# Kernel tuning notes

Measured on AMD Instinct MI355X. Metric: run time of the kernel, lower is better.

## Reference

```python
import jax, jax.numpy as jnp
import numpy as np

C_IN = 64       # in_channels
D = 2 * C_IN    # inner dim d = 128
D4 = 4 * D      # 4-direction SSM dim = 512
N = 16          # SSM state size
DR = 4          # delta_rank = ceil(64/16)
K = 3           # d_conv
B_SZ, H, W = 4, 64, 64
LN_EPS = 1e-5


def setup_inputs() -> dict:
    key = jax.random.key(0)
    ks = jax.random.split(key, 8)
    s = lambda k, shape, sc: jax.random.normal(k, shape, jnp.float32) * sc
    x = jax.random.normal(ks[0], (B_SZ, C_IN, H, W), jnp.float32)
    in_proj_w = s(ks[1], (2 * D, C_IN), 0.05)
    in_proj_b = jnp.zeros((2 * D,), jnp.float32)
    conv_w = s(ks[2], (D, 1, K, K), 0.1)          # depthwise OIHW, groups=D
    conv_b = jnp.zeros((D,), jnp.float32)
    x_proj_w = s(ks[3], (DR + 2 * N, D4), 0.05)   # no bias
    delta_proj_w = s(ks[4], (D4, DR), 0.1)
    delta_proj_b = s(ks[5], (D4,), 0.1)
    A_log = jnp.log(jnp.broadcast_to(jnp.arange(1, N + 1, dtype=jnp.float32), (D4, N)))
    D_param = jnp.ones((D4,), jnp.float32)
    ln_g = jnp.ones((D,), jnp.float32)
    ln_b = jnp.zeros((D,), jnp.float32)
    out_proj_w = s(ks[6], (C_IN, D), 0.05)        # no bias
    return dict(x=x, in_proj_w=in_proj_w, in_proj_b=in_proj_b, conv_w=conv_w,
                conv_b=conv_b, x_proj_w=x_proj_w, delta_proj_w=delta_proj_w,
                delta_proj_b=delta_proj_b, A_log=A_log, D_param=D_param,
                ln_g=ln_g, ln_b=ln_b, out_proj_w=out_proj_w)


def _forward(x, in_proj_w, in_proj_b, conv_w, conv_b, x_proj_w, delta_proj_w,
             delta_proj_b, A_log, D_param, ln_g, ln_b, out_proj_w):
    b, c, h, w = x.shape
    l = h * w
    # in_proj on channels-last, split into x-branch and gate z
    xz = jnp.einsum('bchw,ec->bhwe', x, in_proj_w) + in_proj_b   # (b,h,w,2D)
    xs, z = jnp.split(xz, 2, axis=-1)                             # (b,h,w,D) each
    # depthwise conv (padding 1 == SAME for k=3) + SiLU
    xc = xs.transpose(0, 3, 1, 2)                                 # (b,D,h,w)
    xc = jax.lax.conv_general_dilated(
        xc, conv_w, (1, 1), 'SAME', feature_group_count=D,
        dimension_numbers=('NCHW', 'OIHW', 'NCHW')) + conv_b[None, :, None, None]
    xc = jax.nn.silu(xc)
    # 4 scan directions: row-major, col-major, and their reversals
    x1 = xc.reshape(b, D, l)
    x2 = xc.transpose(0, 1, 3, 2).reshape(b, D, l)                # (w h) order
    xf = xc[:, :, ::-1, ::-1]
    x3 = xf.reshape(b, D, l)
    x4 = xf.transpose(0, 1, 3, 2).reshape(b, D, l)
    u = jnp.concatenate([x1, x2, x3, x4], axis=1).transpose(0, 2, 1)  # (b,l,D4)
    # input-dependent SSM params
    x_dbl = u @ x_proj_w.T                                        # (b,l,DR+2N)
    dlt, Bm, Cm = jnp.split(x_dbl, [DR, DR + N], axis=-1)
    delta = jax.nn.softplus(dlt @ delta_proj_w.T + delta_proj_b)  # (b,l,D4)
    A = -jnp.exp(A_log)                                           # (D4,N)
    # selective scan: h_t = exp(delta_t*A)*h_{t-1} + delta_t*B_t*u_t ; y_t = C_t.h_t
    def step(hst, inp):
        d_t, B_t, C_t, u_t = inp                                  # (b,D4),(b,N),(b,N),(b,D4)
        dA = jnp.exp(d_t[:, :, None] * A[None])                   # (b,D4,N)
        hst = dA * hst + (d_t * u_t)[:, :, None] * B_t[:, None, :]
        y = jnp.einsum('bdn,bn->bd', hst, C_t)
        return hst, y
    h0 = jnp.zeros((b, D4, N), x.dtype)
    xs_seq = (delta.transpose(1, 0, 2), Bm.transpose(1, 0, 2),
              Cm.transpose(1, 0, 2), u.transpose(1, 0, 2))
    _, ys = jax.lax.scan(step, h0, xs_seq)                        # (l,b,D4)
    y = ys.transpose(1, 0, 2) + u * D_param                       # (b,l,D4)
    # split directions and undo each scan ordering
    y = y.reshape(b, l, 4, D).transpose(0, 2, 3, 1)               # (b,4,D,l)
    y1 = y[:, 0].reshape(b, D, h, w)
    y2 = y[:, 1].reshape(b, D, w, h).transpose(0, 1, 3, 2)
    y3 = y[:, 2].reshape(b, D, h, w)[:, :, ::-1, ::-1]
    y4 = y[:, 3].reshape(b, D, w, h).transpose(0, 1, 3, 2)[:, :, ::-1, ::-1]
    ysum = (y1 + y2 + y3 + y4).transpose(0, 2, 3, 1)              # (b,h,w,D)
    # LayerNorm over D, gate with silu(z), out projection
    mu = ysum.mean(-1, keepdims=True)
    var = ysum.var(-1, keepdims=True)
    yn = (ysum - mu) / jnp.sqrt(var + LN_EPS) * ln_g + ln_b
    out = (yn * jax.nn.silu(z)) @ out_proj_w.T                    # (b,h,w,C_IN)
    return out.transpose(0, 3, 1, 2)                              # (b,c,h,w)


def reference(x, in_proj_w, in_proj_b, conv_w, conv_b, x_proj_w, delta_proj_w,
              delta_proj_b, A_log, D_param, ln_g, ln_b, out_proj_w):
    return _forward(x, in_proj_w, in_proj_b, conv_w, conv_b, x_proj_w,
                    delta_proj_w, delta_proj_b, A_log, D_param, ln_g, ln_b,
                    out_proj_w)
```

## Files before the change

### kernel.cpp

```cpp
#include <hip/hip_runtime.h>
#include <math.h>


#define LL   4096
#define NCH  128
#define TCH  32

__device__ __forceinline__ int tauf(int t) { return ((t & 63) << 6) | (t >> 6); }

__global__ __launch_bounds__(256) void k_inproj(const float* __restrict__ x,
    const float* __restrict__ W, const float* __restrict__ bias,
    float* __restrict__ xsl, float* __restrict__ zl)
{
    int tid = threadIdx.x;
    int b   = blockIdx.x >> 8;
    int p0  = (blockIdx.x & 255) << 4;
    int e   = tid;

    float wr[64];
    {
        const float4* wrow = (const float4*)(W + (e << 6));
        #pragma unroll
        for (int k = 0; k < 16; ++k) ((float4*)wr)[k] = wrow[k];
    }
    float acc[16];
    float bv = bias[e];
    #pragma unroll
    for (int j = 0; j < 16; ++j) acc[j] = bv;

    const float* xb = x + ((b << 6) << 12) + p0;
    #pragma unroll
    for (int c = 0; c < 64; ++c) {
        const float* xr = xb + (c << 12);
        float w = wr[c];
        #pragma unroll
        for (int j = 0; j < 16; ++j) acc[j] += w * xr[j];
    }

    float* dst = (e < 128) ? xsl : zl;
    int ch = e & 127;
    #pragma unroll
    for (int j = 0; j < 16; ++j)
        dst[(((b << 12) + p0 + j) << 7) + ch] = acc[j];
}

__global__ __launch_bounds__(256) void k_conv(const float* __restrict__ xsl,
    const float* __restrict__ cw, const float* __restrict__ cb,
    float* __restrict__ xcl)
{
    __shared__ float wlds[1152];
    int tid = threadIdx.x;
    for (int i = tid; i < 1152; i += 256) wlds[i] = cw[i];
    int c    = tid & 127, half = tid >> 7;
    int P0   = blockIdx.x << 3;
    int b    = P0 >> 12;
    int p0   = (P0 & 4095) + (half << 2);
    int r    = p0 >> 6, c0 = p0 & 63;
    __syncthreads();

    float w[9];
    #pragma unroll
    for (int k = 0; k < 9; ++k) w[k] = wlds[c * 9 + k];
    float bv = cb[c];
    float acc[4] = {bv, bv, bv, bv};

    #pragma unroll
    for (int dy = -1; dy <= 1; ++dy) {
        int rr = r + dy;
        if ((unsigned)rr < 64u) {
            float v[6];
            #pragma unroll
            for (int o = 0; o < 6; ++o) {
                int cc = c0 + o - 1;
                v[o] = ((unsigned)cc < 64u)
                     ? xsl[(((b << 12) + (rr << 6) + cc) << 7) + c] : 0.f;
            }
            int wb = (dy + 1) * 3;
            #pragma unroll
            for (int j = 0; j < 4; ++j)
                acc[j] += w[wb] * v[j] + w[wb + 1] * v[j + 1] + w[wb + 2] * v[j + 2];
        }
    }
    #pragma unroll
    for (int j = 0; j < 4; ++j) {
        float a = acc[j];
        xcl[(((b << 12) + p0 + j) << 7) + c] = a / (1.f + __expf(-a));
    }
}

__global__ __launch_bounds__(576) void k_pgemm(const float* __restrict__ xcl,
    const float* __restrict__ xpw, float* __restrict__ P)
{
    __shared__ float ut[16][128];
    __shared__ float res[16][144];
    int tid = threadIdx.x;
    int q4  = tid & 3;
    int jj  = tid >> 2;
    int r0  = blockIdx.x << 4;

    if (tid < 512) {
        int row = tid >> 5, v = tid & 31;
        ((float4*)ut[row])[v] = ((const float4*)xcl)[((r0 + row) << 5) + v];
    }

    int j = jj % 36, g = jj / 36;
    const float4* wrow = (const float4*)(xpw + j * 512 + g * 128 + q4 * 32);
    float4 wreg[8];
    #pragma unroll
    for (int k = 0; k < 8; ++k) wreg[k] = wrow[k];

    __syncthreads();

    #pragma unroll 4
    for (int row = 0; row < 16; ++row) {
        const float4* ur = (const float4*)(ut[row] + q4 * 32);
        float s = 0.f;
        #pragma unroll
        for (int k = 0; k < 8; ++k) {
            float4 u4 = ur[k], w4 = wreg[k];
            s += u4.x * w4.x + u4.y * w4.y + u4.z * w4.z + u4.w * w4.w;
        }
        s += __shfl_xor(s, 1);
        s += __shfl_xor(s, 2);
        if (q4 == 0) res[row][jj] = s;
    }
    __syncthreads();

    #pragma unroll
    for (int k = 0; k < 4; ++k) {
        int idx = tid + k * 576;
        int row = idx / 144, c = idx - row * 144;
        P[(r0 + row) * 144 + c] = res[row][c];
    }
}

__global__ __launch_bounds__(256) void k_xcomb(const float* __restrict__ P,
    const float* __restrict__ dpw, const float* __restrict__ dpb,
    float* __restrict__ delta, float* __restrict__ Bm, float* __restrict__ Cm)
{
    __shared__ float xdb[8][36];
    int tid = threadIdx.x;
    int b   = blockIdx.x >> 9;
    int t0  = (blockIdx.x & 511) << 3;

    for (int i = tid; i < 288; i += 256) {
        int tt = i / 36, j = i - tt * 36;
        int t  = t0 + tt, ta = tauf(t);
        int r0 = (b << 12) + t,        r1 = (b << 12) + ta;
        int r2 = (b << 12) + 4095 - t, r3 = (b << 12) + 4095 - ta;
        float s = P[r0 * 144 + j]       + P[r1 * 144 + 36 + j]
                + P[r2 * 144 + 72 + j]  + P[r3 * 144 + 108 + j];
        xdb[tt][j] = s;
        if (j >= 20)      Cm[((r0) << 4) + j - 20] = s;
        else if (j >= 4)  Bm[((r0) << 4) + j - 4]  = s;
    }
    __syncthreads();

    #pragma unroll
    for (int k = 0; k < 16; ++k) {
        int i  = tid + (k << 8);
        int tt = i >> 9, d = i & 511;
        int t  = t0 + tt;
        float d0 = xdb[tt][0], d1 = xdb[tt][1], d2 = xdb[tt][2], d3 = xdb[tt][3];
        const float4 w = *(const float4*)(dpw + (d << 2));
        float a  = dpb[d] + d0 * w.x + d1 * w.y + d2 * w.z + d3 * w.w;
        float sp = fmaxf(a, 0.f) + log1pf(__expf(-fabsf(a)));
        delta[(((b << 12) + t) << 9) + d] = sp;
    }
}

__global__ __launch_bounds__(256) void k_scanA(const float* __restrict__ delta,
    const float* __restrict__ xcl, const float* __restrict__ Bm,
    const float* __restrict__ Alog,
    float* __restrict__ hloc, float* __restrict__ Ssum)
{
    int tid  = threadIdx.x;
    int half = blockIdx.x & 1;
    int bc   = blockIdx.x >> 1;
    int b = bc >> 7, chunk = bc & 127;
    int d = (half << 8) + tid;
    int g = d >> 7, cd = d & 127;

    float A[16], h[16];
    #pragma unroll
    for (int n = 0; n < 16; ++n) { A[n] = -__expf(Alog[(d << 4) + n]); h[n] = 0.f; }
    float S = 0.f;
    int t0 = chunk << 5;
    for (int t = t0; t < t0 + TCH; ++t) {
        int base = (b << 12) + t;
        float dl = delta[(base << 9) + d];
        int ta  = tauf(t);
        int pos = (g == 0) ? t : (g == 1) ? ta : (g == 2) ? (4095 - t) : (4095 - ta);
        float uv = dl * xcl[(((b << 12) + pos) << 7) + cd];
        const float4* Br = (const float4*)(Bm + (base << 4));
        float4 B0 = Br[0], B1 = Br[1], B2 = Br[2], B3 = Br[3];
        float Bv[16] = {B0.x,B0.y,B0.z,B0.w, B1.x,B1.y,B1.z,B1.w,
                        B2.x,B2.y,B2.z,B2.w, B3.x,B3.y,B3.z,B3.w};
        S += dl;
        #pragma unroll
        for (int n = 0; n < 16; ++n)
            h[n] = __expf(dl * A[n]) * h[n] + uv * Bv[n];
    }
    float4* ho = (float4*)(hloc + ((((b << 9) + d) * NCH + chunk) << 4));
    ho[0] = make_float4(h[0], h[1], h[2], h[3]);
    ho[1] = make_float4(h[4], h[5], h[6], h[7]);
    ho[2] = make_float4(h[8], h[9], h[10], h[11]);
    ho[3] = make_float4(h[12], h[13], h[14], h[15]);
    Ssum[((b << 9) + d) * NCH + chunk] = S;
}

__global__ __launch_bounds__(256) void k_comb(float* __restrict__ hloc,
    const float* __restrict__ Ssum, const float* __restrict__ Alog)
{
    int gidx = blockIdx.x * 256 + threadIdx.x;
    int n  = gidx & 15;
    int bd = gidx >> 4;
    int d  = bd & 511;
    float A = -__expf(Alog[(d << 4) + n]);
    float H = 0.f;
    for (int c0 = 0; c0 < NCH; c0 += 16) {
        float hl[16], ef[16];
        #pragma unroll
        for (int j = 0; j < 16; ++j) {
            hl[j] = hloc[((bd * NCH + c0 + j) << 4) + n];
            ef[j] = Ssum[bd * NCH + c0 + j];
        }
        #pragma unroll
        for (int j = 0; j < 16; ++j) ef[j] = __expf(A * ef[j]);
        #pragma unroll
        for (int j = 0; j < 16; ++j) {
            hloc[((bd * NCH + c0 + j) << 4) + n] = H;
            H = ef[j] * H + hl[j];
        }
    }
}

__global__ __launch_bounds__(256) void k_scanB(const float* __restrict__ delta,
    const float* __restrict__ xcl, const float* __restrict__ Bm,
    const float* __restrict__ Cm, const float* __restrict__ Alog,
    const float* __restrict__ hstart, float* __restrict__ yb)
{
    int tid  = threadIdx.x;
    int half = blockIdx.x & 1;
    int bc   = blockIdx.x >> 1;
    int b = bc >> 7, chunk = bc & 127;
    int d = (half << 8) + tid;
    int g = d >> 7, cd = d & 127;

    float A[16], h[16];
    #pragma unroll
    for (int n = 0; n < 16; ++n) A[n] = -__expf(Alog[(d << 4) + n]);
    const float4* hi = (const float4*)(hstart + ((((b << 9) + d) * NCH + chunk) << 4));
    float4 h0 = hi[0], h1 = hi[1], h2 = hi[2], h3 = hi[3];
    h[0]=h0.x; h[1]=h0.y; h[2]=h0.z; h[3]=h0.w;
    h[4]=h1.x; h[5]=h1.y; h[6]=h1.z; h[7]=h1.w;
    h[8]=h2.x; h[9]=h2.y; h[10]=h2.z; h[11]=h2.w;
    h[12]=h3.x; h[13]=h3.y; h[14]=h3.z; h[15]=h3.w;

    int t0 = chunk << 5;
    for (int t = t0; t < t0 + TCH; ++t) {
        int base = (b << 12) + t;
        float dl = delta[(base << 9) + d];
        int ta  = tauf(t);
        int pos = (g == 0) ? t : (g == 1) ? ta : (g == 2) ? (4095 - t) : (4095 - ta);
        float uv = dl * xcl[(((b << 12) + pos) << 7) + cd];
        const float4* Br = (const float4*)(Bm + (base << 4));
        const float4* Cr = (const float4*)(Cm + (base << 4));
        float4 B0 = Br[0], B1 = Br[1], B2 = Br[2], B3 = Br[3];
        float4 C0 = Cr[0], C1 = Cr[1], C2 = Cr[2], C3 = Cr[3];
        float Bv[16] = {B0.x,B0.y,B0.z,B0.w, B1.x,B1.y,B1.z,B1.w,
                        B2.x,B2.y,B2.z,B2.w, B3.x,B3.y,B3.z,B3.w};
        float Cv[16] = {C0.x,C0.y,C0.z,C0.w, C1.x,C1.y,C1.z,C1.w,
                        C2.x,C2.y,C2.z,C2.w, C3.x,C3.y,C3.z,C3.w};
        float y = 0.f;
        #pragma unroll
        for (int n = 0; n < 16; ++n) {
            h[n] = __expf(dl * A[n]) * h[n] + uv * Bv[n];
            y += h[n] * Cv[n];
        }
        yb[(base << 9) + d] = y;
    }
}

__global__ __launch_bounds__(256) void k_final(const float* __restrict__ yb,
    const float* __restrict__ xcl, const float* __restrict__ zl,
    const float* __restrict__ Dp, const float* __restrict__ lg,
    const float* __restrict__ lb, const float* __restrict__ Wout,
    float* __restrict__ out)
{
    __shared__ float mt[16][4][36];
    __shared__ float res[64][17];
    int tid = threadIdx.x;
    int b   = blockIdx.x >> 8;
    int p0  = (blockIdx.x & 255) << 4;
    int wv  = tid >> 6, lane = tid & 63;

    int co = tid >> 2, q4 = tid & 3;
    float4 wq[8];
    {
        const float4* wrow = (const float4*)(Wout + (co << 7) + (q4 << 5));
        #pragma unroll
        for (int k = 0; k < 8; ++k) wq[k] = wrow[k];
    }

    #pragma unroll
    for (int q = 0; q < 4; ++q) {
        int pos = (wv << 2) + q;
        int p = p0 + pos;
        int ta = tauf(p);
        int base0 = ((b << 12) + p) << 9;
        int base1 = ((b << 12) + ta) << 9;
        int base2 = ((b << 12) + 4095 - p) << 9;
        int base3 = ((b << 12) + 4095 - ta) << 9;

        float v[2]; float s = 0.f, s2 = 0.f;
        #pragma unroll
        for (int k = 0; k < 2; ++k) {
            int dd = lane + (k << 6);
            float vv = yb[base0 + dd]
                     + yb[base1 + 128 + dd]
                     + yb[base2 + 256 + dd]
                     + yb[base3 + 384 + dd]
                     + xcl[(((b << 12) + p) << 7) + dd]
                       * (Dp[dd] + Dp[128 + dd] + Dp[256 + dd] + Dp[384 + dd]);
            v[k] = vv; s += vv; s2 += vv * vv;
        }
        #pragma unroll
        for (int o = 32; o; o >>= 1) { s += __shfl_xor(s, o); s2 += __shfl_xor(s2, o); }
        float mu   = s * (1.f / 128.f);
        float var  = s2 * (1.f / 128.f) - mu * mu;
        float rstd = rsqrtf(var + 1e-5f);
        #pragma unroll
        for (int k = 0; k < 2; ++k) {
            int dd = lane + (k << 6);
            float yn = (v[k] - mu) * rstd * lg[dd] + lb[dd];
            float zz = zl[(((b << 12) + p) << 7) + dd];
            mt[pos][dd >> 5][dd & 31] = yn * (zz / (1.f + __expf(-zz)));
        }
    }
    __syncthreads();

    #pragma unroll 4
    for (int pos = 0; pos < 16; ++pos) {
        const float* mq = &mt[pos][q4][0];
        float s = 0.f;
        #pragma unroll
        for (int k = 0; k < 8; ++k) {
            float4 m4 = *(const float4*)&mq[k << 2];
            float4 w4 = wq[k];
            s += m4.x * w4.x + m4.y * w4.y + m4.z * w4.z + m4.w * w4.w;
        }
        s += __shfl_xor(s, 1);
        s += __shfl_xor(s, 2);
        if (q4 == 0) res[co][pos] = s;
    }
    __syncthreads();

    {
        int co2 = tid >> 2, part = tid & 3;
        float4 o4;
        o4.x = res[co2][(part << 2) + 0];
        o4.y = res[co2][(part << 2) + 1];
        o4.z = res[co2][(part << 2) + 2];
        o4.w = res[co2][(part << 2) + 3];
        *(float4*)&out[(((b << 6) + co2) << 12) + p0 + (part << 2)] = o4;
    }
}

extern "C" void kernel_launch(void* const* d_in, const int* in_sizes, int n_in,
                              void* d_out, int out_size, void* d_ws, size_t ws_size,
                              hipStream_t stream)
{
    const float* x    = (const float*)d_in[0];
    const float* ipw  = (const float*)d_in[1];
    const float* ipb  = (const float*)d_in[2];
    const float* cw   = (const float*)d_in[3];
    const float* cb   = (const float*)d_in[4];
    const float* xpw  = (const float*)d_in[5];
    const float* dpw  = (const float*)d_in[6];
    const float* dpb  = (const float*)d_in[7];
    const float* Alog = (const float*)d_in[8];
    const float* Dp   = (const float*)d_in[9];
    const float* lg   = (const float*)d_in[10];
    const float* lb   = (const float*)d_in[11];
    const float* wout = (const float*)d_in[12];

    float* ws    = (float*)d_ws;
    float* xsl   = ws;
    float* zl    = xsl  + 2097152;
    float* xcl   = zl   + 2097152;
    float* delta = xcl  + 2097152;
    float* Bmb   = delta + 8388608;
    float* Cmb   = Bmb  + 262144;
    float* yb    = Cmb  + 262144;
    float* hloc  = yb   + 8388608;
    float* Ssum  = hloc + 4194304;
    float* Pbuf  = yb;

    float* out = (float*)d_out;

    hipLaunchKernelGGL(k_inproj, dim3(1024), dim3(256), 0, stream, x, ipw, ipb, xsl, zl);
    hipLaunchKernelGGL(k_conv,   dim3(2048), dim3(256), 0, stream, xsl, cw, cb, xcl);
    hipLaunchKernelGGL(k_pgemm,  dim3(1024), dim3(576), 0, stream, xcl, xpw, Pbuf);
    hipLaunchKernelGGL(k_xcomb,  dim3(2048), dim3(256), 0, stream, Pbuf, dpw, dpb,
                       delta, Bmb, Cmb);
    hipLaunchKernelGGL(k_scanA,  dim3(1024), dim3(256), 0, stream, delta, xcl, Bmb,
                       Alog, hloc, Ssum);
    hipLaunchKernelGGL(k_comb,   dim3(128),  dim3(256), 0, stream, hloc, Ssum, Alog);
    hipLaunchKernelGGL(k_scanB,  dim3(1024), dim3(256), 0, stream, delta, xcl, Bmb,
                       Cmb, Alog, hloc, yb);
    hipLaunchKernelGGL(k_final,  dim3(1024), dim3(256), 0, stream, yb, xcl, zl, Dp,
                       lg, lb, wout, out);
}
```

Before: 265.4 us.

## Recompute delta inside scan kernels instead of materializing full delta tensor

The delta projection and softplus move out of the combine kernel and into both scan passes. The full-size delta buffer is no longer written and then read twice; the scans recompute it from a compact 36-float-per-timestep buffer that also carries B and C. The cost is that softplus and a small dot product are computed in both scanA and scanB. The final kernel also hoists the loop-invariant D-sum and LayerNorm gamma/beta loads out of its position loop.

```diff
diff --git a/kernel.cpp b/kernel.cpp
--- a/kernel.cpp
+++ b/kernel.cpp
@@ -134,44 +134,26 @@
     }
 }
 
-__global__ __launch_bounds__(256) void k_xcomb(const float* __restrict__ P,
-    const float* __restrict__ dpw, const float* __restrict__ dpb,
-    float* __restrict__ delta, float* __restrict__ Bm, float* __restrict__ Cm)
-{
-    __shared__ float xdb[8][36];
+__global__ __launch_bounds__(256) void k_xdb(const float* __restrict__ P,
+    float* __restrict__ xdb)
+{
     int tid = threadIdx.x;
-    int b   = blockIdx.x >> 9;
-    int t0  = (blockIdx.x & 511) << 3;
-
-    for (int i = tid; i < 288; i += 256) {
+    int b   = blockIdx.x >> 6;
+    int t0  = (blockIdx.x & 63) << 6;
+    for (int i = tid; i < 64 * 36; i += 256) {
         int tt = i / 36, j = i - tt * 36;
         int t  = t0 + tt, ta = tauf(t);
         int r0 = (b << 12) + t,        r1 = (b << 12) + ta;
         int r2 = (b << 12) + 4095 - t, r3 = (b << 12) + 4095 - ta;
-        float s = P[r0 * 144 + j]       + P[r1 * 144 + 36 + j]
-                + P[r2 * 144 + 72 + j]  + P[r3 * 144 + 108 + j];
-        xdb[tt][j] = s;
-        if (j >= 20)      Cm[((r0) << 4) + j - 20] = s;
-        else if (j >= 4)  Bm[((r0) << 4) + j - 4]  = s;
-    }
-    __syncthreads();
-
-    #pragma unroll
-    for (int k = 0; k < 16; ++k) {
-        int i  = tid + (k << 8);
-        int tt = i >> 9, d = i & 511;
-        int t  = t0 + tt;
-        float d0 = xdb[tt][0], d1 = xdb[tt][1], d2 = xdb[tt][2], d3 = xdb[tt][3];
-        const float4 w = *(const float4*)(dpw + (d << 2));
-        float a  = dpb[d] + d0 * w.x + d1 * w.y + d2 * w.z + d3 * w.w;
-        float sp = fmaxf(a, 0.f) + log1pf(__expf(-fabsf(a)));
-        delta[(((b << 12) + t) << 9) + d] = sp;
-    }
-}
-
-__global__ __launch_bounds__(256) void k_scanA(const float* __restrict__ delta,
-    const float* __restrict__ xcl, const float* __restrict__ Bm,
-    const float* __restrict__ Alog,
+        xdb[(size_t)((b << 12) + t) * 36 + j] =
+              P[r0 * 144 + j]      + P[r1 * 144 + 36 + j]
+            + P[r2 * 144 + 72 + j] + P[r3 * 144 + 108 + j];
+    }
+}
+
+__global__ __launch_bounds__(256) void k_scanA(const float* __restrict__ xdb,
+    const float* __restrict__ xcl, const float* __restrict__ dpw,
+    const float* __restrict__ dpb, const float* __restrict__ Alog,
     float* __restrict__ hloc, float* __restrict__ Ssum)
 {
     int tid  = threadIdx.x;
@@ -184,16 +166,22 @@
     float A[16], h[16];
     #pragma unroll
     for (int n = 0; n < 16; ++n) { A[n] = -__expf(Alog[(d << 4) + n]); h[n] = 0.f; }
+    const float4 w4d = *(const float4*)(dpw + (d << 2));
+    const float dpbv = dpb[d];
     float S = 0.f;
     int t0 = chunk << 5;
     for (int t = t0; t < t0 + TCH; ++t) {
-        int base = (b << 12) + t;
-        float dl = delta[(base << 9) + d];
+        const float* xr = xdb + (size_t)((b << 12) + t) * 36;
+        float4 dt4 = *(const float4*)xr;
+        float a  = dpbv + dt4.x * w4d.x + dt4.y * w4d.y + dt4.z * w4d.z + dt4.w * w4d.w;
+        float dl = fmaxf(a, 0.f) + log1pf(__expf(-fabsf(a)));
         int ta  = tauf(t);
         int pos = (g == 0) ? t : (g == 1) ? ta : (g == 2) ? (4095 - t) : (4095 - ta);
         float uv = dl * xcl[(((b << 12) + pos) << 7) + cd];
-        const float4* Br = (const float4*)(Bm + (base << 4));
-        float4 B0 = Br[0], B1 = Br[1], B2 = Br[2], B3 = Br[3];
+        float4 B0 = *(const float4*)(xr + 4);
+        float4 B1 = *(const float4*)(xr + 8);
+        float4 B2 = *(const float4*)(xr + 12);
+        float4 B3 = *(const float4*)(xr + 16);
         float Bv[16] = {B0.x,B0.y,B0.z,B0.w, B1.x,B1.y,B1.z,B1.w,
                         B2.x,B2.y,B2.z,B2.w, B3.x,B3.y,B3.z,B3.w};
         S += dl;
@@ -235,9 +223,9 @@
     }
 }
 
-__global__ __launch_bounds__(256) void k_scanB(const float* __restrict__ delta,
-    const float* __restrict__ xcl, const float* __restrict__ Bm,
-    const float* __restrict__ Cm, const float* __restrict__ Alog,
+__global__ __launch_bounds__(256) void k_scanB(const float* __restrict__ xdb,
+    const float* __restrict__ xcl, const float* __restrict__ dpw,
+    const float* __restrict__ dpb, const float* __restrict__ Alog,
     const float* __restrict__ hstart, float* __restrict__ yb)
 {
     int tid  = threadIdx.x;
@@ -256,18 +244,26 @@
     h[4]=h1.x; h[5]=h1.y; h[6]=h1.z; h[7]=h1.w;
     h[8]=h2.x; h[9]=h2.y; h[10]=h2.z; h[11]=h2.w;
     h[12]=h3.x; h[13]=h3.y; h[14]=h3.z; h[15]=h3.w;
+    const float4 w4d = *(const float4*)(dpw + (d << 2));
+    const float dpbv = dpb[d];
 
     int t0 = chunk << 5;
     for (int t = t0; t < t0 + TCH; ++t) {
-        int base = (b << 12) + t;
-        float dl = delta[(base << 9) + d];
+        const float* xr = xdb + (size_t)((b << 12) + t) * 36;
+        float4 dt4 = *(const float4*)xr;
+        float a  = dpbv + dt4.x * w4d.x + dt4.y * w4d.y + dt4.z * w4d.z + dt4.w * w4d.w;
+        float dl = fmaxf(a, 0.f) + log1pf(__expf(-fabsf(a)));
         int ta  = tauf(t);
         int pos = (g == 0) ? t : (g == 1) ? ta : (g == 2) ? (4095 - t) : (4095 - ta);
         float uv = dl * xcl[(((b << 12) + pos) << 7) + cd];
-        const float4* Br = (const float4*)(Bm + (base << 4));
-        const float4* Cr = (const float4*)(Cm + (base << 4));
-        float4 B0 = Br[0], B1 = Br[1], B2 = Br[2], B3 = Br[3];
-        float4 C0 = Cr[0], C1 = Cr[1], C2 = Cr[2], C3 = Cr[3];
+        float4 B0 = *(const float4*)(xr + 4);
+        float4 B1 = *(const float4*)(xr + 8);
+        float4 B2 = *(const float4*)(xr + 12);
+        float4 B3 = *(const float4*)(xr + 16);
+        float4 C0 = *(const float4*)(xr + 20);
+        float4 C1 = *(const float4*)(xr + 24);
+        float4 C2 = *(const float4*)(xr + 28);
+        float4 C3 = *(const float4*)(xr + 32);
         float Bv[16] = {B0.x,B0.y,B0.z,B0.w, B1.x,B1.y,B1.z,B1.w,
                         B2.x,B2.y,B2.z,B2.w, B3.x,B3.y,B3.z,B3.w};
         float Cv[16] = {C0.x,C0.y,C0.z,C0.w, C1.x,C1.y,C1.z,C1.w,
@@ -278,7 +274,7 @@
             h[n] = __expf(dl * A[n]) * h[n] + uv * Bv[n];
             y += h[n] * Cv[n];
         }
-        yb[(base << 9) + d] = y;
+        yb[(size_t)(((b << 12) + t) << 9) + d] = y;
     }
 }
 
@@ -301,6 +297,15 @@
         const float4* wrow = (const float4*)(Wout + (co << 7) + (q4 << 5));
         #pragma unroll
         for (int k = 0; k < 8; ++k) wq[k] = wrow[k];
+    }
+
+    float dsum[2], lgv[2], lbv[2];
+    #pragma unroll
+    for (int k = 0; k < 2; ++k) {
+        int dd = lane + (k << 6);
+        dsum[k] = Dp[dd] + Dp[128 + dd] + Dp[256 + dd] + Dp[384 + dd];
+        lgv[k]  = lg[dd];
+        lbv[k]  = lb[dd];
     }
 
     #pragma unroll
@@ -321,8 +326,7 @@
                      + yb[base1 + 128 + dd]
                      + yb[base2 + 256 + dd]
                      + yb[base3 + 384 + dd]
-                     + xcl[(((b << 12) + p) << 7) + dd]
-                       * (Dp[dd] + Dp[128 + dd] + Dp[256 + dd] + Dp[384 + dd]);
+                     + xcl[(((b << 12) + p) << 7) + dd] * dsum[k];
             v[k] = vv; s += vv; s2 += vv * vv;
         }
         #pragma unroll
@@ -333,7 +337,7 @@
         #pragma unroll
         for (int k = 0; k < 2; ++k) {
             int dd = lane + (k << 6);
-            float yn = (v[k] - mu) * rstd * lg[dd] + lb[dd];
+            float yn = (v[k] - mu) * rstd * lgv[k] + lbv[k];
             float zz = zl[(((b << 12) + p) << 7) + dd];
             mt[pos][dd >> 5][dd & 31] = yn * (zz / (1.f + __expf(-zz)));
         }
@@ -389,12 +393,10 @@
     float* xsl   = ws;
     float* zl    = xsl  + 2097152;
     float* xcl   = zl   + 2097152;
-    float* delta = xcl  + 2097152;
-    float* Bmb   = delta + 8388608;
-    float* Cmb   = Bmb  + 262144;
-    float* yb    = Cmb  + 262144;
+    float* yb    = xcl  + 2097152;
     float* hloc  = yb   + 8388608;
     float* Ssum  = hloc + 4194304;
+    float* xdb   = Ssum + 262144;
     float* Pbuf  = yb;
 
     float* out = (float*)d_out;
@@ -402,13 +404,12 @@
     hipLaunchKernelGGL(k_inproj, dim3(1024), dim3(256), 0, stream, x, ipw, ipb, xsl, zl);
     hipLaunchKernelGGL(k_conv,   dim3(2048), dim3(256), 0, stream, xsl, cw, cb, xcl);
     hipLaunchKernelGGL(k_pgemm,  dim3(1024), dim3(576), 0, stream, xcl, xpw, Pbuf);
-    hipLaunchKernelGGL(k_xcomb,  dim3(2048), dim3(256), 0, stream, Pbuf, dpw, dpb,
-                       delta, Bmb, Cmb);
-    hipLaunchKernelGGL(k_scanA,  dim3(1024), dim3(256), 0, stream, delta, xcl, Bmb,
-                       Alog, hloc, Ssum);
+    hipLaunchKernelGGL(k_xdb,    dim3(256),  dim3(256), 0, stream, Pbuf, xdb);
+    hipLaunchKernelGGL(k_scanA,  dim3(1024), dim3(256), 0, stream, xdb, xcl, dpw,
+                       dpb, Alog, hloc, Ssum);
     hipLaunchKernelGGL(k_comb,   dim3(128),  dim3(256), 0, stream, hloc, Ssum, Alog);
-    hipLaunchKernelGGL(k_scanB,  dim3(1024), dim3(256), 0, stream, delta, xcl, Bmb,
-                       Cmb, Alog, hloc, yb);
+    hipLaunchKernelGGL(k_scanB,  dim3(1024), dim3(256), 0, stream, xdb, xcl, dpw,
+                       dpb, Alog, hloc, yb);
     hipLaunchKernelGGL(k_final,  dim3(1024), dim3(256), 0, stream, yb, xcl, zl, Dp,
                        lg, lb, wout, out);
 }
```

New measurement: 290.0 us. 9.2% more time.
